# Kernel optimization log

Hardware: AMD Instinct MI355X
Metric: run time of the kernel (lower is better)

The kernel has to match this reference:

```python
import jax, jax.numpy as jnp
import numpy as np


def setup_inputs() -> dict:
    key = jax.random.key(0)
    k1, k2, k3, kw, kb = jax.random.split(key, 5)
    B, N, M, O, A = 16384, 64, 64, 64, 128  # batch, in1, in2, in3, out
    bound = 1.0 / np.sqrt(N)
    return {
        "input1": jax.random.normal(k1, (B, N), dtype=jnp.float32),
        "input2": jax.random.normal(k2, (B, M), dtype=jnp.float32),
        "input3": jax.random.normal(k3, (B, O), dtype=jnp.float32),
        "weight": jax.random.uniform(kw, (A, N, M, O), dtype=jnp.float32, minval=-bound, maxval=bound),
        "bias": jax.random.uniform(kb, (A,), dtype=jnp.float32, minval=-bound, maxval=bound),
    }


def reference(input1, input2, input3, weight, bias):
    # y[b,a] = sum_{n,m,o} x1[b,n] x2[b,m] x3[b,o] W[a,n,m,o] + bias[a]
    # Explicit low-memory contraction path (avoids any [B,A,n,m] blowup):
    xmo = jnp.einsum('bm,bo->bmo', input2, input3)        # [B, M, O]
    t = jnp.einsum('bmo,anmo->ban', xmo, weight)          # [B, A, N]
    return jnp.einsum('bn,ban->ba', input1, t) + bias     # [B, A]
```

## Files before the change

kernel.cpp:

```cpp
#include <hip/hip_runtime.h>
#include <hip/hip_bf16.h>
#include <stdint.h>

#define AS1 __attribute__((address_space(1)))
#define AS3 __attribute__((address_space(3)))

typedef short s16x8 __attribute__((ext_vector_type(8)));
typedef float f32x16 __attribute__((ext_vector_type(16)));
typedef __bf16 bf16x8_t __attribute__((ext_vector_type(8)));

union ABFrag { bf16x8_t h; s16x8 s; };

__device__ __forceinline__ ushort f2b_rne(float f){
  uint32_t u = __float_as_uint(f);
  u += 0x7fffu + ((u >> 16) & 1u);
  return (ushort)(u >> 16);
}

__global__ __launch_bounds__(256) void pack_w_kernel(const float* __restrict__ W,
                                                     ushort* __restrict__ wsp){
  const int u  = blockIdx.x * 256 + threadIdx.x;
  const int a  = u & 127;
  const int nm = u >> 7;
  const int n  = nm >> 6;
  const int m  = nm & 63;
  const float* src = W + ((size_t)a << 18) + ((size_t)n << 12) + ((size_t)m << 6);
  ushort* dst = wsp + (size_t)nm * 8192;
  const int wn = a >> 5, la = a & 31;
  #pragma unroll
  for (int s = 0; s < 4; ++s){
    #pragma unroll
    for (int g = 0; g < 2; ++g){
      const float4 f0 = *(const float4*)(src + s*16 + g*8);
      const float4 f1 = *(const float4*)(src + s*16 + g*8 + 4);
      uint4 o;
      o.x = (uint32_t)f2b_rne(f0.x) | ((uint32_t)f2b_rne(f0.y) << 16);
      o.y = (uint32_t)f2b_rne(f0.z) | ((uint32_t)f2b_rne(f0.w) << 16);
      o.z = (uint32_t)f2b_rne(f1.x) | ((uint32_t)f2b_rne(f1.y) << 16);
      o.w = (uint32_t)f2b_rne(f1.z) | ((uint32_t)f2b_rne(f1.w) << 16);
      *(uint4*)(dst + (s*4 + wn)*512 + (g*32 + la)*8) = o;
    }
  }
}

__global__ __launch_bounds__(512, 2) void trilinear_gemm_kernel(
    const float* __restrict__ x1g, const float* __restrict__ x2g,
    const float* __restrict__ x3g, const ushort* __restrict__ wsp,
    const float* __restrict__ biasg, float* __restrict__ outg){

  __shared__ __align__(16) char Bbuf[4 * 16384];
  __shared__ ushort x2s[512 * 64];
  __shared__ ushort x1s[512 * 8];

  const int tid  = threadIdx.x;
  const int wave = tid >> 6;
  const int lane = tid & 63;
  const int la   = lane & 31;
  const int lg   = lane >> 5;

  const int bid    = blockIdx.x;
  const int nsplit = bid & 7;
  const int row0   = (bid >> 3) * 512;
  const int n0     = nsplit * 8;

  #pragma unroll
  for (int j = 0; j < 64; ++j){
    const int e = tid + 512 * j;
    const int r = e >> 6, c = e & 63;
    x2s[r*64 + ((c + r) & 63)] = f2b_rne(x2g[(size_t)row0*64 + e]);
  }
  #pragma unroll
  for (int j = 0; j < 8; ++j){
    const int e = tid + 512 * j;
    const int r = e >> 3, c = e & 7;
    x1s[e] = f2b_rne(x1g[(size_t)(row0 + r)*64 + n0 + c]);
  }

  uint32_t x3p[2][16];
  #pragma unroll
  for (int g = 0; g < 2; ++g){
    const int arow = row0 + wave*64 + g*32 + la;
    #pragma unroll
    for (int s = 0; s < 4; ++s){
      const float4 p0 = *(const float4*)(x3g + (size_t)arow*64 + s*16 + lg*8);
      const float4 p1 = *(const float4*)(x3g + (size_t)arow*64 + s*16 + lg*8 + 4);
      x3p[g][s*4+0] = (uint32_t)f2b_rne(p0.x) | ((uint32_t)f2b_rne(p0.y) << 16);
      x3p[g][s*4+1] = (uint32_t)f2b_rne(p0.z) | ((uint32_t)f2b_rne(p0.w) << 16);
      x3p[g][s*4+2] = (uint32_t)f2b_rne(p1.x) | ((uint32_t)f2b_rne(p1.y) << 16);
      x3p[g][s*4+3] = (uint32_t)f2b_rne(p1.z) | ((uint32_t)f2b_rne(p1.w) << 16);
    }
  }

  f32x16 acc[2][4];
  #pragma unroll
  for (int g = 0; g < 2; ++g)
    #pragma unroll
    for (int wn = 0; wn < 4; ++wn) acc[g][wn] = 0.f;

  const ushort* wbase = wsp + (size_t)n0 * 64 * 8192;

  #pragma unroll
  for (int pb = 0; pb < 2; ++pb){
    const char* sp = (const char*)wbase + (size_t)pb*16384 + wave*2048 + lane*16;
    char* dp = Bbuf + pb*16384 + wave*2048;
    __builtin_amdgcn_global_load_lds((const AS1 uint32_t*)sp,        (AS3 uint32_t*)dp,        16, 0, 0);
    __builtin_amdgcn_global_load_lds((const AS1 uint32_t*)(sp+1024), (AS3 uint32_t*)(dp+1024), 16, 0, 0);
  }
  __syncthreads();

  const int rl0 = wave*64 + la;
  const int rl1 = rl0 + 32;

  for (int t = 0; t < 512; ++t){
    {
      const int nb = (t + 2) & 511;
      const char* sp = (const char*)wbase + (size_t)nb*16384 + wave*2048 + lane*16;
      char* dp = Bbuf + ((t + 2) & 3)*16384 + wave*2048;
      __builtin_amdgcn_global_load_lds((const AS1 uint32_t*)sp,        (AS3 uint32_t*)dp,        16, 0, 0);
      __builtin_amdgcn_global_load_lds((const AS1 uint32_t*)(sp+1024), (AS3 uint32_t*)(dp+1024), 16, 0, 0);
    }
    asm volatile("s_waitcnt vmcnt(4)\n\ts_barrier" ::: "memory");

    const int m  = t & 63;
    const int nc = t >> 6;
    const float c0 = __uint_as_float((uint32_t)x1s[rl0*8 + nc] << 16) *
                     __uint_as_float((uint32_t)x2s[rl0*64 + ((m + rl0) & 63)] << 16);
    const float c1 = __uint_as_float((uint32_t)x1s[rl1*8 + nc] << 16) *
                     __uint_as_float((uint32_t)x2s[rl1*64 + ((m + rl1) & 63)] << 16);

    const char* bb = Bbuf + (t & 3)*16384 + (lane << 4);
    #pragma unroll
    for (int s = 0; s < 4; ++s){
      ABFrag a0, a1;
      #pragma unroll
      for (int j = 0; j < 8; ++j){
        const uint32_t u0 = x3p[0][s*4 + (j >> 1)];
        const uint32_t u1 = x3p[1][s*4 + (j >> 1)];
        const float v0 = __uint_as_float((j & 1) ? (u0 & 0xFFFF0000u) : (u0 << 16));
        const float v1 = __uint_as_float((j & 1) ? (u1 & 0xFFFF0000u) : (u1 << 16));
        a0.h[j] = (__bf16)(c0 * v0);
        a1.h[j] = (__bf16)(c1 * v1);
      }
      #pragma unroll
      for (int wn = 0; wn < 4; ++wn){
        const s16x8 bf = *(const s16x8*)(bb + ((s*4 + wn) << 10));
        acc[0][wn] = __builtin_amdgcn_mfma_f32_32x32x16_bf16(a0.s, bf, acc[0][wn], 0, 0, 0);
        acc[1][wn] = __builtin_amdgcn_mfma_f32_32x32x16_bf16(a1.s, bf, acc[1][wn], 0, 0, 0);
      }
    }
  }

  #pragma unroll
  for (int g = 0; g < 2; ++g){
    #pragma unroll
    for (int wn = 0; wn < 4; ++wn){
      const int col = wn*32 + la;
      const float bv = (nsplit == 0) ? biasg[col] : 0.f;
      #pragma unroll
      for (int r = 0; r < 16; ++r){
        const int row = row0 + wave*64 + g*32 + (r & 3) + 8*(r >> 2) + 4*lg;
        atomicAdd(outg + (size_t)row*128 + col, acc[g][wn][r] + bv);
      }
    }
  }
}

extern "C" void kernel_launch(void* const* d_in, const int* in_sizes, int n_in,
                              void* d_out, int out_size, void* d_ws, size_t ws_size,
                              hipStream_t stream){
  const float* x1   = (const float*)d_in[0];
  const float* x2   = (const float*)d_in[1];
  const float* x3   = (const float*)d_in[2];
  const float* W    = (const float*)d_in[3];
  const float* bias = (const float*)d_in[4];
  float* out = (float*)d_out;

  hipMemsetAsync(d_out, 0, (size_t)16384 * 128 * sizeof(float), stream);

  if (ws_size < (size_t)64 * 1024 * 1024) return;

  ushort* wsp = (ushort*)d_ws;
  pack_w_kernel<<<2048, 256, 0, stream>>>(W, wsp);
  trilinear_gemm_kernel<<<256, 512, 0, stream>>>(x1, x2, x3, wsp, bias, out);
}
```

Before: 1.087 ms.

## Switch operands to fp16 with packed multiplies and LDS-staged weight packing

Moves all operands from bf16 to fp16. This makes the per-step A-fragment build a set of packed f16x2 multiplies instead of scalar float multiplies with bf16 rounding, and the MFMA becomes the f16 variant. The weight pack kernel now runs one block per (n,m) pair and stages 128x64 weights through swizzled LDS, so global writes are contiguous 16-byte chunks. x1 is stored transposed in LDS. The risk is fp16 overflow or precision loss: the x1*x2 product is formed in half precision, and values outside the fp16 range could saturate.

```diff
diff --git a/kernel.cpp b/kernel.cpp
--- a/kernel.cpp
+++ b/kernel.cpp
@@ -5,41 +5,49 @@
 #define AS1 __attribute__((address_space(1)))
 #define AS3 __attribute__((address_space(3)))
 
-typedef short s16x8 __attribute__((ext_vector_type(8)));
+typedef _Float16 f16x8 __attribute__((ext_vector_type(8)));
+typedef _Float16 f16x2 __attribute__((ext_vector_type(2)));
 typedef float f32x16 __attribute__((ext_vector_type(16)));
-typedef __bf16 bf16x8_t __attribute__((ext_vector_type(8)));
 
-union ABFrag { bf16x8_t h; s16x8 s; };
+union AF { f16x8 v; f16x2 p[4]; };
 
-__device__ __forceinline__ ushort f2b_rne(float f){
-  uint32_t u = __float_as_uint(f);
-  u += 0x7fffu + ((u >> 16) & 1u);
-  return (ushort)(u >> 16);
+__device__ __forceinline__ ushort f2h(float f){
+  union { _Float16 h; ushort u; } cv; cv.h = (_Float16)f; return cv.u;
+}
+__device__ __forceinline__ _Float16 u2h(ushort u){
+  union { _Float16 h; ushort u; } cv; cv.u = u; return cv.h;
 }
 
 __global__ __launch_bounds__(256) void pack_w_kernel(const float* __restrict__ W,
                                                      ushort* __restrict__ wsp){
-  const int u  = blockIdx.x * 256 + threadIdx.x;
-  const int a  = u & 127;
-  const int nm = u >> 7;
-  const int n  = nm >> 6;
-  const int m  = nm & 63;
-  const float* src = W + ((size_t)a << 18) + ((size_t)n << 12) + ((size_t)m << 6);
+  __shared__ ushort lds[128 * 64];
+  const int nm  = blockIdx.x;
+  const int n   = nm >> 6;
+  const int m   = nm & 63;
+  const int tid = threadIdx.x;
+  const float* src = W + ((size_t)n << 12) + ((size_t)m << 6);
+
+  #pragma unroll
+  for (int j = 0; j < 32; ++j){
+    const int e = tid + 256 * j;
+    const int a = e >> 6, o = e & 63;
+    const float v = src[((size_t)a << 18) + o];
+    lds[a*64 + (o ^ ((a & 7) << 3))] = f2h(v);
+  }
+  __syncthreads();
+
   ushort* dst = wsp + (size_t)nm * 8192;
-  const int wn = a >> 5, la = a & 31;
   #pragma unroll
-  for (int s = 0; s < 4; ++s){
-    #pragma unroll
-    for (int g = 0; g < 2; ++g){
-      const float4 f0 = *(const float4*)(src + s*16 + g*8);
-      const float4 f1 = *(const float4*)(src + s*16 + g*8 + 4);
-      uint4 o;
-      o.x = (uint32_t)f2b_rne(f0.x) | ((uint32_t)f2b_rne(f0.y) << 16);
-      o.y = (uint32_t)f2b_rne(f0.z) | ((uint32_t)f2b_rne(f0.w) << 16);
-      o.z = (uint32_t)f2b_rne(f1.x) | ((uint32_t)f2b_rne(f1.y) << 16);
-      o.w = (uint32_t)f2b_rne(f1.z) | ((uint32_t)f2b_rne(f1.w) << 16);
-      *(uint4*)(dst + (s*4 + wn)*512 + (g*32 + la)*8) = o;
-    }
+  for (int j = 0; j < 4; ++j){
+    const int c  = tid + 256 * j;
+    const int f  = c >> 6;
+    const int q  = c & 63;
+    const int wn = f & 3, s = f >> 2;
+    const int g  = q >> 5, la = q & 31;
+    const int a  = wn*32 + la;
+    const int o0 = s*16 + g*8;
+    *(uint4*)(dst + (size_t)c * 8) =
+        *(const uint4*)(lds + a*64 + (o0 ^ ((a & 7) << 3)));
   }
 }
 
@@ -50,7 +58,7 @@
 
   __shared__ __align__(16) char Bbuf[4 * 16384];
   __shared__ ushort x2s[512 * 64];
-  __shared__ ushort x1s[512 * 8];
+  __shared__ ushort x1s[8 * 512];
 
   const int tid  = threadIdx.x;
   const int wave = tid >> 6;
@@ -67,16 +75,13 @@
   for (int j = 0; j < 64; ++j){
     const int e = tid + 512 * j;
     const int r = e >> 6, c = e & 63;
-    x2s[r*64 + ((c + r) & 63)] = f2b_rne(x2g[(size_t)row0*64 + e]);
+    x2s[r*64 + ((c + r) & 63)] = f2h(x2g[(size_t)row0*64 + e]);
   }
   #pragma unroll
-  for (int j = 0; j < 8; ++j){
-    const int e = tid + 512 * j;
-    const int r = e >> 3, c = e & 7;
-    x1s[e] = f2b_rne(x1g[(size_t)(row0 + r)*64 + n0 + c]);
-  }
+  for (int j = 0; j < 8; ++j)
+    x1s[j*512 + tid] = f2h(x1g[(size_t)(row0 + tid)*64 + n0 + j]);
 
-  uint32_t x3p[2][16];
+  f16x2 x3h[2][16];
   #pragma unroll
   for (int g = 0; g < 2; ++g){
     const int arow = row0 + wave*64 + g*32 + la;
@@ -84,10 +89,10 @@
     for (int s = 0; s < 4; ++s){
       const float4 p0 = *(const float4*)(x3g + (size_t)arow*64 + s*16 + lg*8);
       const float4 p1 = *(const float4*)(x3g + (size_t)arow*64 + s*16 + lg*8 + 4);
-      x3p[g][s*4+0] = (uint32_t)f2b_rne(p0.x) | ((uint32_t)f2b_rne(p0.y) << 16);
-      x3p[g][s*4+1] = (uint32_t)f2b_rne(p0.z) | ((uint32_t)f2b_rne(p0.w) << 16);
-      x3p[g][s*4+2] = (uint32_t)f2b_rne(p1.x) | ((uint32_t)f2b_rne(p1.y) << 16);
-      x3p[g][s*4+3] = (uint32_t)f2b_rne(p1.z) | ((uint32_t)f2b_rne(p1.w) << 16);
+      x3h[g][s*4+0] = f16x2{(_Float16)p0.x, (_Float16)p0.y};
+      x3h[g][s*4+1] = f16x2{(_Float16)p0.z, (_Float16)p0.w};
+      x3h[g][s*4+2] = f16x2{(_Float16)p1.x, (_Float16)p1.y};
+      x3h[g][s*4+3] = f16x2{(_Float16)p1.z, (_Float16)p1.w};
     }
   }
 
@@ -123,29 +128,25 @@
 
     const int m  = t & 63;
     const int nc = t >> 6;
-    const float c0 = __uint_as_float((uint32_t)x1s[rl0*8 + nc] << 16) *
-                     __uint_as_float((uint32_t)x2s[rl0*64 + ((m + rl0) & 63)] << 16);
-    const float c1 = __uint_as_float((uint32_t)x1s[rl1*8 + nc] << 16) *
-                     __uint_as_float((uint32_t)x2s[rl1*64 + ((m + rl1) & 63)] << 16);
+    const _Float16 h0 = u2h(x1s[nc*512 + rl0]) * u2h(x2s[rl0*64 + ((m + rl0) & 63)]);
+    const _Float16 h1 = u2h(x1s[nc*512 + rl1]) * u2h(x2s[rl1*64 + ((m + rl1) & 63)]);
+    const f16x2 hc0 = {h0, h0};
+    const f16x2 hc1 = {h1, h1};
 
     const char* bb = Bbuf + (t & 3)*16384 + (lane << 4);
     #pragma unroll
     for (int s = 0; s < 4; ++s){
-      ABFrag a0, a1;
+      AF a0, a1;
       #pragma unroll
-      for (int j = 0; j < 8; ++j){
-        const uint32_t u0 = x3p[0][s*4 + (j >> 1)];
-        const uint32_t u1 = x3p[1][s*4 + (j >> 1)];
-        const float v0 = __uint_as_float((j & 1) ? (u0 & 0xFFFF0000u) : (u0 << 16));
-        const float v1 = __uint_as_float((j & 1) ? (u1 & 0xFFFF0000u) : (u1 << 16));
-        a0.h[j] = (__bf16)(c0 * v0);
-        a1.h[j] = (__bf16)(c1 * v1);
+      for (int jj = 0; jj < 4; ++jj){
+        a0.p[jj] = hc0 * x3h[0][s*4 + jj];
+        a1.p[jj] = hc1 * x3h[1][s*4 + jj];
       }
       #pragma unroll
       for (int wn = 0; wn < 4; ++wn){
-        const s16x8 bf = *(const s16x8*)(bb + ((s*4 + wn) << 10));
-        acc[0][wn] = __builtin_amdgcn_mfma_f32_32x32x16_bf16(a0.s, bf, acc[0][wn], 0, 0, 0);
-        acc[1][wn] = __builtin_amdgcn_mfma_f32_32x32x16_bf16(a1.s, bf, acc[1][wn], 0, 0, 0);
+        const f16x8 bf = *(const f16x8*)(bb + ((s*4 + wn) << 10));
+        acc[0][wn] = __builtin_amdgcn_mfma_f32_32x32x16_f16(a0.v, bf, acc[0][wn], 0, 0, 0);
+        acc[1][wn] = __builtin_amdgcn_mfma_f32_32x32x16_f16(a1.v, bf, acc[1][wn], 0, 0, 0);
       }
     }
   }
@@ -180,6 +181,6 @@
   if (ws_size < (size_t)64 * 1024 * 1024) return;
 
   ushort* wsp = (ushort*)d_ws;
-  pack_w_kernel<<<2048, 256, 0, stream>>>(W, wsp);
+  pack_w_kernel<<<4096, 256, 0, stream>>>(W, wsp);
   trilinear_gemm_kernel<<<256, 512, 0, stream>>>(x1, x2, x3, wsp, bias, out);
 }
```

Result: faster. 1.030 ms (-5.3%).
